# Performance work log

Measured on AMD Instinct MI355X. Metric: run time of the kernel, lower is better.

Reference implementation:

```python
import jax, jax.numpy as jnp
import numpy as np

B, L, N, HID, NH, HD, SH, SW, MH = 1, 512, 2048, 2048, 16, 128, 64, 32, 8192


def _rms(x, w, eps=1e-6):
    return x * jax.lax.rsqrt(jnp.mean(x * x, axis=-1, keepdims=True) + eps) * w


def _adaln(x, emb, W, b, nw):
    e = jax.nn.silu(emb) @ W + b  # [B, 6*hid]
    sh_m, sc_m, g_m, sh_p, sc_p, g_p = jnp.split(e, 6, axis=-1)
    xm = _rms(x, nw) * (1.0 + sc_m[:, None]) + sh_m[:, None]
    return xm, g_m, sh_p, sc_p, g_p


def _rope(x, rope):
    # x: [B, H, S, D], rope: [S, 1, D]
    f = rope[:, 0]  # [S, D]
    cos = jnp.repeat(f[:, 0::2], 2, axis=-1)[None, None]
    sin = jnp.repeat(f[:, 1::2], 2, axis=-1)[None, None]
    xr = x.reshape(*x.shape[:-1], -1, 2)
    x_rot = jnp.stack([-xr[..., 1], xr[..., 0]], axis=-1).reshape(x.shape)
    return x * cos + x_rot * sin


def _sdpa(q, k, v, scale):
    s = jnp.einsum('bhqd,bhkd->bhqk', q, k) * scale
    return jnp.einsum('bhqk,bhkd->bhqd', jax.nn.softmax(s, axis=-1), v)


def _mlp(x, w1, b1, w2, b2):
    return jax.nn.gelu(x @ w1 + b1, approximate=True) @ w2 + b2


def setup_inputs() -> dict:
    key = jax.random.key(0)
    ks = iter(jax.random.split(key, 32))
    r = lambda *s: jax.random.normal(next(ks), s, dtype=jnp.float32) * 0.02
    inp = {
        'txt': jax.random.normal(next(ks), (B, L, HID), dtype=jnp.float32),
        'img': jax.random.normal(next(ks), (B, N, HID), dtype=jnp.float32),
        'vec': jax.random.normal(next(ks), (B, HID), dtype=jnp.float32),
        'rope': jax.random.normal(next(ks), (N, 1, HD), dtype=jnp.float32),
        'sol_temperature': jax.random.uniform(next(ks), (B, 64), dtype=jnp.float32),
        'sol_spatial': jax.random.normal(next(ks), (B, 8, 8), dtype=jnp.float32),
        'ada_img_w': r(HID, 6 * HID), 'ada_img_b': jnp.zeros(6 * HID, jnp.float32), 'ada_img_nw': jnp.ones(HID, jnp.float32),
        'ada_txt_w': r(HID, 6 * HID), 'ada_txt_b': jnp.zeros(6 * HID, jnp.float32), 'ada_txt_nw': jnp.ones(HID, jnp.float32),
        'txt_qkv_w': r(HID, 3 * HID), 'img_qkv_w': r(HID, 3 * HID),
        'txt_out_w': r(HID, HID), 'img_out_w': r(HID, HID),
        'mod_w': r(NH) * 5.0, 'mod_b': r(NH) * 5.0,
        'img_n2_w': jnp.ones(HID, jnp.float32), 'txt_n2_w': jnp.ones(HID, jnp.float32),
        'img_fc1_w': r(HID, MH), 'img_fc1_b': jnp.zeros(MH, jnp.float32),
        'img_fc2_w': r(MH, HID), 'img_fc2_b': jnp.zeros(HID, jnp.float32),
        'txt_fc1_w': r(HID, MH), 'txt_fc1_b': jnp.zeros(MH, jnp.float32),
        'txt_fc2_w': r(MH, HID), 'txt_fc2_b': jnp.zeros(HID, jnp.float32),
        'spatial_h': SH, 'spatial_w': SW,
    }
    return inp


def reference(txt, img, vec, rope, sol_temperature, sol_spatial,
              ada_img_w, ada_img_b, ada_img_nw, ada_txt_w, ada_txt_b, ada_txt_nw,
              txt_qkv_w, img_qkv_w, txt_out_w, img_out_w, mod_w, mod_b,
              img_n2_w, txt_n2_w, img_fc1_w, img_fc1_b, img_fc2_w, img_fc2_b,
              txt_fc1_w, txt_fc1_b, txt_fc2_w, txt_fc2_b, spatial_h, spatial_w):
    b, l, hid = txt.shape
    n = img.shape[1]
    nh = mod_w.shape[0]
    hd = hid // nh
    scale = hd ** (-0.5)

    img_n, img_g, img_shp, img_scp, img_gp = _adaln(img, vec, ada_img_w, ada_img_b, ada_img_nw)
    txt_n, txt_g, txt_shp, txt_scp, txt_gp = _adaln(txt, vec, ada_txt_w, ada_txt_b, ada_txt_nw)

    def qkv(x, w, s):
        p = (x @ w).reshape(b, s, 3, nh, hd).transpose(2, 0, 3, 1, 4)  # [3,B,H,S,D]
        return p[0], p[1], p[2]

    tq, tk, tv = qkv(txt_n, txt_qkv_w, l)
    iq, ik, iv = qkv(img_n, img_qkv_w, n)
    iq = _rope(iq, rope)
    ik = _rope(ik, rope)

    # SOL spatial modulation: bilinear upsample (align_corners=False) + 1x1 conv + exp(clamp)
    sol_up = jax.image.resize(sol_spatial, (b, spatial_h, spatial_w), 'bilinear')
    mod = sol_up[:, None] * mod_w[None, :, None, None] + mod_b[None, :, None, None]
    mod = jnp.exp(jnp.clip(mod, -2.0, 2.0)).reshape(b, nh, n, 1)
    iq = iq * mod
    ik = ik * mod

    k = jnp.concatenate([tk, ik], axis=2)  # [B,H,L+N,D]
    v = jnp.concatenate([tv, iv], axis=2)

    txt_attn = _sdpa(tq, k, v, scale).transpose(0, 2, 1, 3).reshape(b, l, hid) @ txt_out_w

    temp = jnp.clip(jnp.mean(sol_temperature, axis=1, keepdims=True), 0.1)  # [B,1]
    s_eff = jnp.sqrt(scale / temp)[:, :, None, None]  # [B,1,1,1]
    img_attn = _sdpa(iq * s_eff, k * s_eff, v, 1.0).transpose(0, 2, 1, 3).reshape(b, n, hid) @ img_out_w

    txt = txt + txt_g[:, None] * txt_attn
    img = img + img_g[:, None] * img_attn

    txt_in = _rms(txt, txt_n2_w) * (1.0 + txt_scp[:, None]) + txt_shp[:, None]
    img_in = _rms(img, img_n2_w) * (1.0 + img_scp[:, None]) + img_shp[:, None]
    txt = txt + txt_gp[:, None] * _mlp(txt_in, txt_fc1_w, txt_fc1_b, txt_fc2_w, txt_fc2_b)
    img = img + img_gp[:, None] * _mlp(img_in, img_fc1_w, img_fc1_b, img_fc2_w, img_fc2_b)
    return txt, img
```

## Files before the change

kernel.cpp:

```cpp
#include <hip/hip_runtime.h>

typedef short short8 __attribute__((ext_vector_type(8)));
typedef float f32x4 __attribute__((ext_vector_type(4)));

__device__ __forceinline__ unsigned short f2bu(float f) {
  unsigned u = __builtin_bit_cast(unsigned, f);
  u += 0x7fffu + ((u >> 16) & 1u);
  return (unsigned short)(u >> 16);
}

__device__ __forceinline__ float b2f(unsigned short b) {
  unsigned u = (unsigned)b << 16;
  return __builtin_bit_cast(float, u);
}

__device__ __forceinline__ float gelu_t(float x) {
  float x3 = x * x * x;
  float t = tanhf(0.7978845608028654f * (x + 0.044715f * x3));
  return 0.5f * x * (1.f + t);
}

__device__ __forceinline__ void gload16(const void* g, void* l) {
  __builtin_amdgcn_global_load_lds(
      (const __attribute__((address_space(1))) void*)g,
      (__attribute__((address_space(3))) void*)l, 16, 0, 0);
}

__global__ __launch_bounds__(256) void prep_small(
    const float* __restrict__ vec, const float* __restrict__ sol_t,
    float* __restrict__ silu_vec, float* __restrict__ scales) {
  __shared__ float red[4];
  int t = threadIdx.x;
  float v = (t < 64) ? sol_t[t] : 0.f;
#pragma unroll
  for (int o = 32; o > 0; o >>= 1) v += __shfl_down(v, o);
  if ((t & 63) == 0) red[t >> 6] = v;
  __syncthreads();
  if (t == 0) {
    float m = (red[0] + red[1] + red[2] + red[3]) * (1.f / 64.f);
    m = fmaxf(m, 0.1f);
    const float sc = 0.08838834764831845f;
    const float l2e = 1.4426950408889634f;
    scales[0] = sc * l2e;
    scales[1] = sc / m * l2e;
  }
  for (int k = t; k < 2048; k += 256) {
    float x = vec[k];
    silu_vec[k] = x / (1.f + expf(-x));
  }
}

__global__ __launch_bounds__(256) void mod_kernel(
    const float* __restrict__ S, const float* __restrict__ mw,
    const float* __restrict__ mb, float* __restrict__ modb) {
  int idx = blockIdx.x * 256 + threadIdx.x;
  int h = idx >> 11, n = idx & 2047;
  int y = n >> 5, x = n & 31;
  float cy = (y + 0.5f) * 0.125f - 0.5f;
  float cx = (x + 0.5f) * 0.25f - 0.5f;
  int y0 = (int)floorf(cy); float fy = cy - (float)y0;
  int x0 = (int)floorf(cx); float fx = cx - (float)x0;
  int y0c = min(max(y0, 0), 7), y1c = min(max(y0 + 1, 0), 7);
  int x0c = min(max(x0, 0), 7), x1c = min(max(x0 + 1, 0), 7);
  float v = (1.f - fy) * ((1.f - fx) * S[y0c * 8 + x0c] + fx * S[y0c * 8 + x1c]) +
            fy * ((1.f - fx) * S[y1c * 8 + x0c] + fx * S[y1c * 8 + x1c]);
  float t = v * mw[h] + mb[h];
  t = fminf(fmaxf(t, -2.f), 2.f);
  modb[idx] = expf(t);
}

__global__ __launch_bounds__(256) void ada_gemv(
    const float* __restrict__ sv,
    const float* __restrict__ Wi, const float* __restrict__ bi,
    const float* __restrict__ Wt, const float* __restrict__ bt,
    float* __restrict__ ei, float* __restrict__ et) {
  __shared__ float red[4][64];
  const float* W = blockIdx.y ? Wt : Wi;
  const float* bb = blockIdx.y ? bt : bi;
  float* e = blockIdx.y ? et : ei;
  int jl = threadIdx.x & 63, ks = threadIdx.x >> 6;
  int j = blockIdx.x * 64 + jl;
  float acc = 0.f;
  int k0 = ks * 512;
#pragma unroll 4
  for (int k = 0; k < 512; ++k) acc += sv[k0 + k] * W[(size_t)(k0 + k) * 12288 + j];
  red[ks][jl] = acc;
  __syncthreads();
  if (ks == 0) e[j] = red[0][jl] + red[1][jl] + red[2][jl] + red[3][jl] + bb[j];
}

__global__ __launch_bounds__(256) void rmsmod_kernel(
    const float* __restrict__ X, const float* __restrict__ nw,
    const float* __restrict__ e, int sh_off, int sc_off,
    unsigned short* __restrict__ out) {
  __shared__ float red[4];
  int r = blockIdx.x, t = threadIdx.x;
  const float4* xr = reinterpret_cast<const float4*>(X + (size_t)r * 2048);
  float4 v0 = xr[t * 2], v1 = xr[t * 2 + 1];
  float ss = v0.x * v0.x + v0.y * v0.y + v0.z * v0.z + v0.w * v0.w +
             v1.x * v1.x + v1.y * v1.y + v1.z * v1.z + v1.w * v1.w;
#pragma unroll
  for (int o = 32; o > 0; o >>= 1) ss += __shfl_down(ss, o);
  if ((t & 63) == 0) red[t >> 6] = ss;
  __syncthreads();
  float rinv = rsqrtf((red[0] + red[1] + red[2] + red[3]) * (1.f / 2048.f) + 1e-6f);
  int c0 = t * 8;
  float xv[8] = {v0.x, v0.y, v0.z, v0.w, v1.x, v1.y, v1.z, v1.w};
  short8 ov;
#pragma unroll
  for (int i = 0; i < 8; ++i) {
    int c = c0 + i;
    float y = xv[i] * rinv * nw[c] * (1.f + e[sc_off + c]) + e[sh_off + c];
    ov[i] = (short)f2bu(y);
  }
  *reinterpret_cast<short8*>(out + (size_t)r * 2048 + c0) = ov;
}

__global__ __launch_bounds__(256) void transpose_w(
    const float* __restrict__ W, unsigned short* __restrict__ Bt, int K, int N) {
  __shared__ float tile[64][33];
  int n0 = blockIdx.x * 32, k0 = blockIdx.y * 64;
  int tid = threadIdx.x;
  int tx = tid & 31, ty = tid >> 5;
#pragma unroll
  for (int j = 0; j < 8; ++j)
    tile[ty + j * 8][tx] = W[(size_t)(k0 + ty + j * 8) * N + n0 + tx];
  __syncthreads();
  int n = tid >> 3, ks = (tid & 7) * 8;
  unsigned pk[4];
#pragma unroll
  for (int i = 0; i < 4; ++i) {
    float lo = tile[ks + 2 * i][n], hi = tile[ks + 2 * i + 1][n];
    pk[i] = (unsigned)f2bu(lo) | ((unsigned)f2bu(hi) << 16);
  }
  int4 ov = make_int4(pk[0], pk[1], pk[2], pk[3]);
  *reinterpret_cast<int4*>(Bt + (size_t)(n0 + n) * K + k0 + ks) = ov;
}

__global__ __launch_bounds__(256) void transpose_v(
    const unsigned short* __restrict__ V, unsigned short* __restrict__ Vt) {
  __shared__ unsigned short tile[32][33];
  int h = blockIdx.z;
  int s0 = blockIdx.x * 32, d0 = blockIdx.y * 32;
  int tx = threadIdx.x, ty = threadIdx.y;
  const unsigned short* src = V + (size_t)h * 2560 * 128;
  unsigned short* dst = Vt + (size_t)h * 128 * 2560;
#pragma unroll
  for (int j = 0; j < 32; j += 8)
    tile[ty + j][tx] = src[(size_t)(s0 + ty + j) * 128 + d0 + tx];
  __syncthreads();
#pragma unroll
  for (int j = 0; j < 32; j += 8)
    dst[(size_t)(d0 + ty + j) * 2560 + s0 + tx] = tile[tx][ty + j];
}

struct GemmP {
  const unsigned short *A, *Bt_t, *Bt_i;
  float* C;
  unsigned short* Cb;
  const float *bias_t, *bias_i;
  const float *rope, *modb;
  unsigned short *q_txt, *q_img, *k_cat, *v_cat;
  const float* scales;
  int Mb_t;
  int N, K, KS;
};

template <int EPI>
__global__ __launch_bounds__(256) void gemm2(GemmP p) {
  __shared__ int4 sA[2][128 * 8];
  __shared__ int4 sB[2][128 * 8];
  const int NB = gridDim.x, MBT = gridDim.y;
  int nwg = NB * MBT;
  int orig = blockIdx.y * NB + blockIdx.x;
  int qq = nwg >> 3, rr = nwg & 7, xcd = orig & 7, base = orig >> 3;
  int sw = (xcd < rr ? xcd * (qq + 1) : rr * (qq + 1) + (xcd - rr) * qq) + base;
  int bx = sw / MBT, by = sw % MBT;
  const bool is_t = by < p.Mb_t;
  const unsigned short* Bt = is_t ? p.Bt_t : p.Bt_i;
  const int m0 = by * 128, n0 = bx * 128;
  const int z = blockIdx.z;
  const int Kz = p.K / p.KS, kbeg = z * Kz, kend = kbeg + Kz;
  const int tid = threadIdx.x;
  const int w = tid >> 6, l = tid & 63, lr = l & 15, lg = l >> 4;
  const int wm = (w >> 1) * 64, wn = (w & 1) * 64;
  f32x4 acc[4][4] = {};
  const int4* Ag = reinterpret_cast<const int4*>(p.A);
  const int4* Bg = reinterpret_cast<const int4*>(Bt);
  const int K8 = p.K >> 3;
  int srow[4], sch[4];
#pragma unroll
  for (int i = 0; i < 4; ++i) {
    int s = i * 256 + tid;
    srow[i] = s >> 3;
    sch[i] = (s & 7) ^ (srow[i] & 7);
  }
  {
    int kc = kbeg >> 3;
#pragma unroll
    for (int i = 0; i < 4; ++i) {
      gload16(&Ag[(size_t)(m0 + srow[i]) * K8 + kc + sch[i]], &sA[0][i * 256 + w * 64]);
      gload16(&Bg[(size_t)(n0 + srow[i]) * K8 + kc + sch[i]], &sB[0][i * 256 + w * 64]);
    }
  }
  asm volatile("s_waitcnt vmcnt(0)" ::: "memory");
  __builtin_amdgcn_sched_barrier(0);
  __builtin_amdgcn_s_barrier();
  int cur = 0;
  for (int k0 = kbeg; k0 < kend; k0 += 64) {
    if (k0 + 64 < kend) {
      int kc = (k0 + 64) >> 3;
#pragma unroll
      for (int i = 0; i < 4; ++i) {
        gload16(&Ag[(size_t)(m0 + srow[i]) * K8 + kc + sch[i]], &sA[cur ^ 1][i * 256 + w * 64]);
        gload16(&Bg[(size_t)(n0 + srow[i]) * K8 + kc + sch[i]], &sB[cur ^ 1][i * 256 + w * 64]);
      }
      __builtin_amdgcn_sched_barrier(0);
    }
    const short8* pA = reinterpret_cast<const short8*>(sA[cur]);
    const short8* pB = reinterpret_cast<const short8*>(sB[cur]);
#pragma unroll
    for (int kk = 0; kk < 2; ++kk) {
      short8 af[4], bf[4];
#pragma unroll
      for (int m = 0; m < 4; ++m) {
        int row = wm + m * 16 + lr;
        af[m] = pA[row * 8 + ((kk * 4 + lg) ^ (row & 7))];
      }
#pragma unroll
      for (int n = 0; n < 4; ++n) {
        int row = wn + n * 16 + lr;
        bf[n] = pB[row * 8 + ((kk * 4 + lg) ^ (row & 7))];
      }
#pragma unroll
      for (int m = 0; m < 4; ++m)
#pragma unroll
        for (int n = 0; n < 4; ++n)
          acc[m][n] = __builtin_amdgcn_mfma_f32_16x16x32_bf16(af[m], bf[n], acc[m][n], 0, 0, 0);
    }
    asm volatile("s_waitcnt vmcnt(0)" ::: "memory");
    __builtin_amdgcn_sched_barrier(0);
    __builtin_amdgcn_s_barrier();
    cur ^= 1;
  }
  if (EPI == 0) {
    float* C = p.C + (size_t)z * MBT * 128 * p.N;
#pragma unroll
    for (int m = 0; m < 4; ++m)
#pragma unroll
      for (int n = 0; n < 4; ++n)
#pragma unroll
        for (int j = 0; j < 4; ++j) {
          int r = m0 + wm + m * 16 + lg * 4 + j;
          int cc = n0 + wn + n * 16 + lr;
          C[(size_t)r * p.N + cc] = acc[m][n][j];
        }
  } else if (EPI == 1) {
    const float* bias = is_t ? p.bias_t : p.bias_i;
#pragma unroll
    for (int n = 0; n < 4; ++n) {
      int cc = n0 + wn + n * 16 + lr;
      float bv = bias[cc];
#pragma unroll
      for (int m = 0; m < 4; ++m)
#pragma unroll
        for (int j = 0; j < 4; ++j) {
          int r = m0 + wm + m * 16 + lg * 4 + j;
          p.Cb[(size_t)r * p.N + cc] = f2bu(gelu_t(acc[m][n][j] + bv));
        }
    }
  } else {
    int sel = bx >> 4, h = bx & 15;
#pragma unroll
    for (int n = 0; n < 4; ++n) {
      int d = wn + n * 16 + lr;
#pragma unroll
      for (int m = 0; m < 4; ++m)
#pragma unroll
        for (int j = 0; j < 4; ++j) {
          int r = m0 + wm + m * 16 + lg * 4 + j;
          float v = acc[m][n][j];
          if (is_t) {
            if (sel == 0) p.q_txt[((size_t)h * 512 + r) * 128 + d] = f2bu(v * p.scales[0]);
            else if (sel == 1) p.k_cat[((size_t)h * 2560 + r) * 128 + d] = f2bu(v);
            else p.v_cat[((size_t)h * 2560 + r) * 128 + d] = f2bu(v);
          } else {
            int s = r - 512;
            if (sel == 2) {
              p.v_cat[((size_t)h * 2560 + r) * 128 + d] = f2bu(v);
            } else {
              float c = p.rope[s * 128 + (d & ~1)];
              float sn = p.rope[s * 128 + (d | 1)];
              float part = __shfl_xor(v, 1);
              float vr = (d & 1) ? v * c + part * sn : v * c - part * sn;
              vr *= p.modb[h * 2048 + s];
              if (sel == 0) p.q_img[((size_t)h * 2048 + s) * 128 + d] = f2bu(vr * p.scales[1]);
              else p.k_cat[((size_t)h * 2560 + r) * 128 + d] = f2bu(vr);
            }
          }
        }
    }
  }
}

__global__ __launch_bounds__(256, 4) void attn_kernel(
    const unsigned short* __restrict__ q_txt, const unsigned short* __restrict__ q_img,
    const unsigned short* __restrict__ Kc, const unsigned short* __restrict__ Vt,
    unsigned short* __restrict__ Op, float* __restrict__ ml) {
  __shared__ __align__(16) char RAW[40960];
  int4* sK = reinterpret_cast<int4*>(RAW);
  int4* sV = reinterpret_cast<int4*>(RAW + 16384);
  int4* sP = reinterpret_cast<int4*>(RAW + 32768);
  unsigned short* osh = reinterpret_cast<unsigned short*>(RAW);
  const int tid = threadIdx.x, w = tid >> 6, l = tid & 63, lr = l & 15, lg = l >> 4;
  const int bx = blockIdx.x, h = blockIdx.y, z = blockIdx.z;
  const bool is_t = bx < 8;
  const int orow = is_t ? bx * 64 : 512 + (bx - 8) * 64;
  const unsigned short* Qp = is_t ? q_txt + ((size_t)h * 512 + bx * 64) * 128
                                  : q_img + ((size_t)h * 2048 + (bx - 8) * 64) * 128;
  short8 aq[4];
#pragma unroll
  for (int ds = 0; ds < 4; ++ds) {
    int row = w * 16 + lr;
    aq[ds] = *reinterpret_cast<const short8*>(Qp + (size_t)row * 128 + ds * 32 + lg * 8);
  }
  const int4* Kg = reinterpret_cast<const int4*>(Kc + (size_t)h * 2560 * 128);
  const int4* Vg = reinterpret_cast<const int4*>(Vt + (size_t)h * 128 * 2560);
  const short8* pK = reinterpret_cast<const short8*>(sK);
  const short8* pV = reinterpret_cast<const short8*>(sV);
  const short8* pP = reinterpret_cast<const short8*>(sP);
  unsigned short* sPb = reinterpret_cast<unsigned short*>(sP);
  int krow[4], kch[4], vrow[4], vch[4];
#pragma unroll
  for (int i = 0; i < 4; ++i) {
    int s = i * 256 + tid;
    krow[i] = s >> 4; kch[i] = (s & 15) ^ (krow[i] & 7);
    vrow[i] = s >> 3; vch[i] = (s & 7) ^ (vrow[i] & 7);
  }
  short8 ones8;
#pragma unroll
  for (int i = 0; i < 8; ++i) ones8[i] = (short)0x3F80;

  f32x4 oacc[8] = {};
  f32x4 oacc_l = {};
  float m_run[4];
#pragma unroll
  for (int j = 0; j < 4; ++j) m_run[j] = -1e30f;

  const int kbeg = z * 10, kend = kbeg + 10;
#pragma unroll
  for (int i = 0; i < 4; ++i)
    gload16(&Kg[(size_t)(kbeg * 64 + krow[i]) * 16 + kch[i]], &sK[i * 256 + w * 64]);
#pragma unroll
  for (int i = 0; i < 4; ++i)
    gload16(&Vg[(size_t)vrow[i] * 320 + kbeg * 8 + vch[i]], &sV[i * 256 + w * 64]);

  for (int kt = kbeg; kt < kend; ++kt) {
    asm volatile("s_waitcnt vmcnt(4)" ::: "memory");
    __builtin_amdgcn_sched_barrier(0);
    __builtin_amdgcn_s_barrier();
    f32x4 sacc[4] = {};
    __builtin_amdgcn_s_setprio(1);
#pragma unroll
    for (int ds = 0; ds < 4; ++ds) {
      short8 bk[4];
#pragma unroll
      for (int n = 0; n < 4; ++n) {
        int row = n * 16 + lr;
        bk[n] = pK[row * 16 + ((ds * 4 + lg) ^ (row & 7))];
      }
#pragma unroll
      for (int n = 0; n < 4; ++n)
        sacc[n] = __builtin_amdgcn_mfma_f32_16x16x32_bf16(aq[ds], bk[n], sacc[n], 0, 0, 0);
    }
    __builtin_amdgcn_s_setprio(0);
    __builtin_amdgcn_s_barrier();
    if (kt + 1 < kend) {
#pragma unroll
      for (int i = 0; i < 4; ++i)
        gload16(&Kg[(size_t)((kt + 1) * 64 + krow[i]) * 16 + kch[i]], &sK[i * 256 + w * 64]);
    }
    float corr_[4];
    bool grow_any = false;
#pragma unroll
    for (int j = 0; j < 4; ++j) {
      float mx = fmaxf(fmaxf(sacc[0][j], sacc[1][j]), fmaxf(sacc[2][j], sacc[3][j]));
      mx = fmaxf(mx, __shfl_xor(mx, 1));
      mx = fmaxf(mx, __shfl_xor(mx, 2));
      mx = fmaxf(mx, __shfl_xor(mx, 4));
      mx = fmaxf(mx, __shfl_xor(mx, 8));
      bool grow = mx > m_run[j] + 11.0f;
      grow_any |= grow;
      float mn = grow ? mx : m_run[j];
      corr_[j] = exp2f(m_run[j] - mn);
      m_run[j] = mn;
      int prow = w * 16 + lg * 4 + j;
#pragma unroll
      for (int n = 0; n < 4; ++n) {
        float pp = exp2f(sacc[n][j] - mn);
        int col = n * 16 + lr;
        sPb[prow * 64 + (((col >> 3) ^ (prow & 7)) << 3) + (col & 7)] = f2bu(pp);
      }
    }
    if (__any(grow_any)) {
#pragma unroll
      for (int n = 0; n < 8; ++n)
#pragma unroll
        for (int j = 0; j < 4; ++j) oacc[n][j] *= corr_[j];
#pragma unroll
      for (int j = 0; j < 4; ++j) oacc_l[j] *= corr_[j];
    }
    if (kt + 1 < kend) {
      asm volatile("s_waitcnt vmcnt(4)" ::: "memory");
    } else {
      asm volatile("s_waitcnt vmcnt(0)" ::: "memory");
    }
    __builtin_amdgcn_sched_barrier(0);
    __builtin_amdgcn_s_barrier();
    __builtin_amdgcn_s_setprio(1);
#pragma unroll
    for (int kk = 0; kk < 2; ++kk) {
      short8 ap, bv[8];
      {
        int row = w * 16 + lr;
        ap = pP[row * 8 + ((kk * 4 + lg) ^ (row & 7))];
      }
#pragma unroll
      for (int n = 0; n < 8; ++n) {
        int row = n * 16 + lr;
        bv[n] = pV[row * 8 + ((kk * 4 + lg) ^ (row & 7))];
      }
#pragma unroll
      for (int n = 0; n < 8; ++n)
        oacc[n] = __builtin_amdgcn_mfma_f32_16x16x32_bf16(ap, bv[n], oacc[n], 0, 0, 0);
      oacc_l = __builtin_amdgcn_mfma_f32_16x16x32_bf16(ap, ones8, oacc_l, 0, 0, 0);
    }
    __builtin_amdgcn_s_setprio(0);
    __builtin_amdgcn_s_barrier();
    if (kt + 1 < kend) {
#pragma unroll
      for (int i = 0; i < 4; ++i)
        gload16(&Vg[(size_t)vrow[i] * 320 + (kt + 1) * 8 + vch[i]], &sV[i * 256 + w * 64]);
    }
  }
  const size_t zbase = (size_t)z * 40960 + (size_t)h * 2560 + orow;
  __syncthreads();
#pragma unroll
  for (int j = 0; j < 4; ++j) {
    int row = w * 16 + lg * 4 + j;
#pragma unroll
    for (int n = 0; n < 8; ++n)
      osh[row * 136 + n * 16 + lr] = f2bu(oacc[n][j]);
    if (lr == 0) {
      ml[(zbase + row) * 2] = m_run[j];
      ml[(zbase + row) * 2 + 1] = oacc_l[j];
    }
  }
  __syncthreads();
  {
    int row = tid >> 2, c0 = (tid & 3) * 32;
#pragma unroll
    for (int i = 0; i < 4; ++i)
      *reinterpret_cast<short8*>(Op + (zbase + row) * 128 + c0 + i * 8) =
          *reinterpret_cast<const short8*>(osh + row * 136 + c0 + i * 8);
  }
}

__global__ __launch_bounds__(256) void attn_merge(
    const unsigned short* __restrict__ Op, const float* __restrict__ ml,
    unsigned short* __restrict__ ao) {
  int gid = blockIdx.x * 256 + threadIdx.x;
  int rid = gid >> 5, d0 = (gid & 31) * 4;
  int h = rid / 2560;
  int r = rid - h * 2560;
  float M = -1e30f;
#pragma unroll
  for (int z = 0; z < 4; ++z) M = fmaxf(M, ml[((size_t)z * 40960 + rid) * 2]);
  float L = 0.f, o0 = 0.f, o1 = 0.f, o2 = 0.f, o3 = 0.f;
#pragma unroll
  for (int z = 0; z < 4; ++z) {
    size_t sidx = (size_t)z * 40960 + rid;
    float mz = ml[sidx * 2], lz = ml[sidx * 2 + 1];
    float wgt = exp2f(mz - M);
    L += wgt * lz;
    ushort4 v = *reinterpret_cast<const ushort4*>(Op + sidx * 128 + d0);
    o0 += wgt * b2f(v.x); o1 += wgt * b2f(v.y);
    o2 += wgt * b2f(v.z); o3 += wgt * b2f(v.w);
  }
  float inv = 1.f / L;
  ushort4 ov;
  ov.x = f2bu(o0 * inv); ov.y = f2bu(o1 * inv);
  ov.z = f2bu(o2 * inv); ov.w = f2bu(o3 * inv);
  *reinterpret_cast<ushort4*>(ao + (size_t)r * 2048 + h * 128 + d0) = ov;
}

__global__ __launch_bounds__(256) void residual1(
    const float4* __restrict__ X, const float4* __restrict__ P0,
    const float4* __restrict__ P1, const float* __restrict__ e,
    float4* __restrict__ out, int total4) {
  int stride = gridDim.x * 256;
  for (int i = blockIdx.x * 256 + threadIdx.x; i < total4; i += stride) {
    int c = (i * 4) & 2047;
    float4 g = *reinterpret_cast<const float4*>(e + 4096 + c);
    float4 x = X[i], p0 = P0[i], p1 = P1[i], o;
    o.x = x.x + g.x * (p0.x + p1.x); o.y = x.y + g.y * (p0.y + p1.y);
    o.z = x.z + g.z * (p0.z + p1.z); o.w = x.w + g.w * (p0.w + p1.w);
    out[i] = o;
  }
}

__global__ __launch_bounds__(256) void residual2(
    const float4* __restrict__ P0, const float4* __restrict__ P1,
    const float* __restrict__ b2, const float* __restrict__ e,
    float4* __restrict__ out, int total4) {
  int stride = gridDim.x * 256;
  for (int i = blockIdx.x * 256 + threadIdx.x; i < total4; i += stride) {
    int c = (i * 4) & 2047;
    float4 g = *reinterpret_cast<const float4*>(e + 10240 + c);
    float4 bb = *reinterpret_cast<const float4*>(b2 + c);
    float4 p0 = P0[i], p1 = P1[i], o = out[i];
    o.x += g.x * (p0.x + p1.x + bb.x); o.y += g.y * (p0.y + p1.y + bb.y);
    o.z += g.z * (p0.z + p1.z + bb.z); o.w += g.w * (p0.w + p1.w + bb.w);
    out[i] = o;
  }
}

extern "C" void kernel_launch(void* const* d_in, const int* in_sizes, int n_in,
                              void* d_out, int out_size, void* d_ws, size_t ws_size,
                              hipStream_t stream) {
  (void)in_sizes; (void)n_in; (void)out_size; (void)ws_size;
  const float* txt = (const float*)d_in[0];
  const float* img = (const float*)d_in[1];
  const float* vec = (const float*)d_in[2];
  const float* rope = (const float*)d_in[3];
  const float* sol_t = (const float*)d_in[4];
  const float* sol_s = (const float*)d_in[5];
  const float* ada_img_w = (const float*)d_in[6];
  const float* ada_img_b = (const float*)d_in[7];
  const float* ada_img_nw = (const float*)d_in[8];
  const float* ada_txt_w = (const float*)d_in[9];
  const float* ada_txt_b = (const float*)d_in[10];
  const float* ada_txt_nw = (const float*)d_in[11];
  const float* txt_qkv_w = (const float*)d_in[12];
  const float* img_qkv_w = (const float*)d_in[13];
  const float* txt_out_w = (const float*)d_in[14];
  const float* img_out_w = (const float*)d_in[15];
  const float* mod_w = (const float*)d_in[16];
  const float* mod_b = (const float*)d_in[17];
  const float* img_n2_w = (const float*)d_in[18];
  const float* txt_n2_w = (const float*)d_in[19];
  const float* img_fc1_w = (const float*)d_in[20];
  const float* img_fc1_b = (const float*)d_in[21];
  const float* img_fc2_w = (const float*)d_in[22];
  const float* img_fc2_b = (const float*)d_in[23];
  const float* txt_fc1_w = (const float*)d_in[24];
  const float* txt_fc1_b = (const float*)d_in[25];
  const float* txt_fc2_w = (const float*)d_in[26];
  const float* txt_fc2_b = (const float*)d_in[27];
  float* out = (float*)d_out;
  float* out_img = out + (size_t)512 * 2048;
  char* ws = (char*)d_ws;

  const size_t MB = 1 << 20;
  float* silu_vec = (float*)(ws + 0);
  float* scales = (float*)(ws + 8192);
  float* modb = (float*)(ws + 16384);
  float* e_img = (float*)(ws + 147456);
  float* e_txt = (float*)(ws + 196608);
  unsigned short* wt0 = (unsigned short*)(ws + 1 * MB);
  unsigned short* wt1 = (unsigned short*)(ws + 33 * MB);
  unsigned short* Opart = (unsigned short*)(ws + 1 * MB);
  float* mlbuf = (float*)(ws + 42 * MB);
  unsigned short* actA = (unsigned short*)(ws + 65 * MB);
  char* attn_base = ws + 75 * MB;
  unsigned short* q_txt = (unsigned short*)(attn_base);
  unsigned short* q_img = (unsigned short*)(attn_base + 2 * MB);
  unsigned short* k_cat = (unsigned short*)(attn_base + 10 * MB);
  unsigned short* v_cat = (unsigned short*)(attn_base + 20 * MB);
  unsigned short* vT = (unsigned short*)(attn_base + 30 * MB);
  unsigned short* ao = (unsigned short*)(attn_base + 40 * MB);
  unsigned short* actB = (unsigned short*)attn_base;
  float* Cbuf = (float*)(ws + 125 * MB);
  const size_t PSTR = (size_t)2560 * 2048;

  prep_small<<<1, 256, 0, stream>>>(vec, sol_t, silu_vec, scales);
  mod_kernel<<<128, 256, 0, stream>>>(sol_s, mod_w, mod_b, modb);
  ada_gemv<<<dim3(192, 2), 256, 0, stream>>>(silu_vec, ada_img_w, ada_img_b,
                                             ada_txt_w, ada_txt_b, e_img, e_txt);
  rmsmod_kernel<<<512, 256, 0, stream>>>(txt, ada_txt_nw, e_txt, 0, 2048, actA);
  rmsmod_kernel<<<2048, 256, 0, stream>>>(img, ada_img_nw, e_img, 0, 2048,
                                          actA + (size_t)512 * 2048);
  transpose_w<<<dim3(192, 32), 256, 0, stream>>>(txt_qkv_w, wt0, 2048, 6144);
  transpose_w<<<dim3(192, 32), 256, 0, stream>>>(img_qkv_w, wt1, 2048, 6144);
  {
    GemmP p = {actA, wt0, wt1, nullptr, nullptr, nullptr, nullptr,
               rope, modb, q_txt, q_img, k_cat, v_cat, scales, 4, 6144, 2048, 1};
    gemm2<2><<<dim3(48, 20, 1), 256, 0, stream>>>(p);
  }
  transpose_v<<<dim3(80, 4, 16), dim3(32, 8), 0, stream>>>(v_cat, vT);
  attn_kernel<<<dim3(40, 16, 4), 256, 0, stream>>>(q_txt, q_img, k_cat, vT, Opart, mlbuf);
  attn_merge<<<5120, 256, 0, stream>>>(Opart, mlbuf, ao);
  transpose_w<<<dim3(64, 32), 256, 0, stream>>>(txt_out_w, wt0, 2048, 2048);
  transpose_w<<<dim3(64, 32), 256, 0, stream>>>(img_out_w, wt1, 2048, 2048);
  {
    GemmP p = {ao, wt0, wt1, Cbuf, nullptr, nullptr, nullptr,
               nullptr, nullptr, nullptr, nullptr, nullptr, nullptr, nullptr, 4, 2048, 2048, 2};
    gemm2<0><<<dim3(16, 20, 2), 256, 0, stream>>>(p);
  }
  residual1<<<512, 256, 0, stream>>>((const float4*)txt, (const float4*)Cbuf,
                                     (const float4*)(Cbuf + PSTR), e_txt,
                                     (float4*)out, 512 * 2048 / 4);
  residual1<<<1024, 256, 0, stream>>>((const float4*)img,
                                      (const float4*)(Cbuf + (size_t)512 * 2048),
                                      (const float4*)(Cbuf + PSTR + (size_t)512 * 2048), e_img,
                                      (float4*)out_img, 2048 * 2048 / 4);
  rmsmod_kernel<<<512, 256, 0, stream>>>(out, txt_n2_w, e_txt, 6144, 8192, actA);
  rmsmod_kernel<<<2048, 256, 0, stream>>>(out_img, img_n2_w, e_img, 6144, 8192,
                                          actA + (size_t)512 * 2048);
  transpose_w<<<dim3(256, 32), 256, 0, stream>>>(txt_fc1_w, wt0, 2048, 8192);
  transpose_w<<<dim3(256, 32), 256, 0, stream>>>(img_fc1_w, wt1, 2048, 8192);
  {
    GemmP p = {actA, wt0, wt1, nullptr, actB, txt_fc1_b, img_fc1_b,
               nullptr, nullptr, nullptr, nullptr, nullptr, nullptr, nullptr, 4, 8192, 2048, 1};
    gemm2<1><<<dim3(64, 20, 1), 256, 0, stream>>>(p);
  }
  transpose_w<<<dim3(64, 128), 256, 0, stream>>>(txt_fc2_w, wt0, 8192, 2048);
  transpose_w<<<dim3(64, 128), 256, 0, stream>>>(img_fc2_w, wt1, 8192, 2048);
  {
    GemmP p = {actB, wt0, wt1, Cbuf, nullptr, nullptr, nullptr,
               nullptr, nullptr, nullptr, nullptr, nullptr, nullptr, nullptr, 4, 2048, 8192, 2};
    gemm2<0><<<dim3(16, 20, 2), 256, 0, stream>>>(p);
  }
  residual2<<<512, 256, 0, stream>>>((const float4*)Cbuf, (const float4*)(Cbuf + PSTR),
                                     txt_fc2_b, e_txt, (float4*)out, 512 * 2048 / 4);
  residual2<<<1024, 256, 0, stream>>>((const float4*)(Cbuf + (size_t)512 * 2048),
                                      (const float4*)(Cbuf + PSTR + (size_t)512 * 2048),
                                      img_fc2_b, e_img, (float4*)out_img, 2048 * 2048 / 4);
}
```

Measured before the change: 853.7 us.

## Stage QKV GEMM epilogue through LDS for vectorized stores; XCD-swizzle attention blocks

```diff
diff --git a/kernel.cpp b/kernel.cpp
--- a/kernel.cpp
+++ b/kernel.cpp
@@ -168,8 +168,9 @@
 
 template <int EPI>
 __global__ __launch_bounds__(256) void gemm2(GemmP p) {
-  __shared__ int4 sA[2][128 * 8];
-  __shared__ int4 sB[2][128 * 8];
+  __shared__ __align__(16) char GRAW[65536];
+  int4* sAb = reinterpret_cast<int4*>(GRAW);
+  int4* sBb = reinterpret_cast<int4*>(GRAW + 32768);
   const int NB = gridDim.x, MBT = gridDim.y;
   int nwg = NB * MBT;
   int orig = blockIdx.y * NB + blockIdx.x;
@@ -199,8 +200,8 @@
     int kc = kbeg >> 3;
 #pragma unroll
     for (int i = 0; i < 4; ++i) {
-      gload16(&Ag[(size_t)(m0 + srow[i]) * K8 + kc + sch[i]], &sA[0][i * 256 + w * 64]);
-      gload16(&Bg[(size_t)(n0 + srow[i]) * K8 + kc + sch[i]], &sB[0][i * 256 + w * 64]);
+      gload16(&Ag[(size_t)(m0 + srow[i]) * K8 + kc + sch[i]], &sAb[i * 256 + w * 64]);
+      gload16(&Bg[(size_t)(n0 + srow[i]) * K8 + kc + sch[i]], &sBb[i * 256 + w * 64]);
     }
   }
   asm volatile("s_waitcnt vmcnt(0)" ::: "memory");
@@ -210,15 +211,16 @@
   for (int k0 = kbeg; k0 < kend; k0 += 64) {
     if (k0 + 64 < kend) {
       int kc = (k0 + 64) >> 3;
+      int nb = (cur ^ 1) * 1024;
 #pragma unroll
       for (int i = 0; i < 4; ++i) {
-        gload16(&Ag[(size_t)(m0 + srow[i]) * K8 + kc + sch[i]], &sA[cur ^ 1][i * 256 + w * 64]);
-        gload16(&Bg[(size_t)(n0 + srow[i]) * K8 + kc + sch[i]], &sB[cur ^ 1][i * 256 + w * 64]);
+        gload16(&Ag[(size_t)(m0 + srow[i]) * K8 + kc + sch[i]], &sAb[nb + i * 256 + w * 64]);
+        gload16(&Bg[(size_t)(n0 + srow[i]) * K8 + kc + sch[i]], &sBb[nb + i * 256 + w * 64]);
       }
       __builtin_amdgcn_sched_barrier(0);
     }
-    const short8* pA = reinterpret_cast<const short8*>(sA[cur]);
-    const short8* pB = reinterpret_cast<const short8*>(sB[cur]);
+    const short8* pA = reinterpret_cast<const short8*>(sAb + cur * 1024);
+    const short8* pB = reinterpret_cast<const short8*>(sBb + cur * 1024);
 #pragma unroll
     for (int kk = 0; kk < 2; ++kk) {
       short8 af[4], bf[4];
@@ -270,35 +272,73 @@
         }
     }
   } else {
+    unsigned short* osh = reinterpret_cast<unsigned short*>(GRAW);
+#pragma unroll
+    for (int m = 0; m < 4; ++m)
+#pragma unroll
+      for (int n = 0; n < 4; ++n)
+#pragma unroll
+        for (int j = 0; j < 4; ++j) {
+          int row = wm + m * 16 + lg * 4 + j;
+          int col = wn + n * 16 + lr;
+          osh[row * 136 + col] = f2bu(acc[m][n][j]);
+        }
+    __syncthreads();
     int sel = bx >> 4, h = bx & 15;
-#pragma unroll
-    for (int n = 0; n < 4; ++n) {
-      int d = wn + n * 16 + lr;
-#pragma unroll
-      for (int m = 0; m < 4; ++m)
-#pragma unroll
-        for (int j = 0; j < 4; ++j) {
-          int r = m0 + wm + m * 16 + lg * 4 + j;
-          float v = acc[m][n][j];
-          if (is_t) {
-            if (sel == 0) p.q_txt[((size_t)h * 512 + r) * 128 + d] = f2bu(v * p.scales[0]);
-            else if (sel == 1) p.k_cat[((size_t)h * 2560 + r) * 128 + d] = f2bu(v);
-            else p.v_cat[((size_t)h * 2560 + r) * 128 + d] = f2bu(v);
-          } else {
-            int s = r - 512;
-            if (sel == 2) {
-              p.v_cat[((size_t)h * 2560 + r) * 128 + d] = f2bu(v);
-            } else {
-              float c = p.rope[s * 128 + (d & ~1)];
-              float sn = p.rope[s * 128 + (d | 1)];
-              float part = __shfl_xor(v, 1);
-              float vr = (d & 1) ? v * c + part * sn : v * c - part * sn;
-              vr *= p.modb[h * 2048 + s];
-              if (sel == 0) p.q_img[((size_t)h * 2048 + s) * 128 + d] = f2bu(vr * p.scales[1]);
-              else p.k_cat[((size_t)h * 2560 + r) * 128 + d] = f2bu(vr);
-            }
+    int row = tid >> 1, d0 = (tid & 1) * 64;
+    int r = m0 + row;
+    const unsigned short* src = osh + row * 136 + d0;
+    if (is_t) {
+      if (sel == 0) {
+        float qs = p.scales[0];
+        unsigned short* dst = p.q_txt + ((size_t)h * 512 + r) * 128 + d0;
+#pragma unroll
+        for (int i = 0; i < 8; ++i) {
+          short8 v = *reinterpret_cast<const short8*>(src + i * 8);
+          short8 o;
+#pragma unroll
+          for (int t = 0; t < 8; ++t)
+            o[t] = (short)f2bu(b2f((unsigned short)v[t]) * qs);
+          *reinterpret_cast<short8*>(dst + i * 8) = o;
+        }
+      } else {
+        unsigned short* dst =
+            (sel == 1 ? p.k_cat : p.v_cat) + ((size_t)h * 2560 + r) * 128 + d0;
+#pragma unroll
+        for (int i = 0; i < 8; ++i)
+          *reinterpret_cast<short8*>(dst + i * 8) =
+              *reinterpret_cast<const short8*>(src + i * 8);
+      }
+    } else {
+      int s = r - 512;
+      if (sel == 2) {
+        unsigned short* dst = p.v_cat + ((size_t)h * 2560 + r) * 128 + d0;
+#pragma unroll
+        for (int i = 0; i < 8; ++i)
+          *reinterpret_cast<short8*>(dst + i * 8) =
+              *reinterpret_cast<const short8*>(src + i * 8);
+      } else {
+        float mv = p.modb[h * 2048 + s];
+        float qs = (sel == 0) ? p.scales[1] * mv : mv;
+        const float2* rp = reinterpret_cast<const float2*>(p.rope + (size_t)s * 128 + d0);
+        unsigned short* dst = (sel == 0)
+            ? p.q_img + ((size_t)h * 2048 + s) * 128 + d0
+            : p.k_cat + ((size_t)h * 2560 + r) * 128 + d0;
+#pragma unroll
+        for (int i = 0; i < 8; ++i) {
+          short8 v = *reinterpret_cast<const short8*>(src + i * 8);
+          short8 o;
+#pragma unroll
+          for (int t = 0; t < 4; ++t) {
+            float2 cs = rp[i * 4 + t];
+            float e = b2f((unsigned short)v[2 * t]);
+            float od = b2f((unsigned short)v[2 * t + 1]);
+            o[2 * t] = (short)f2bu((e * cs.x - od * cs.y) * qs);
+            o[2 * t + 1] = (short)f2bu((od * cs.x + e * cs.y) * qs);
           }
+          *reinterpret_cast<short8*>(dst + i * 8) = o;
         }
+      }
     }
   }
 }
@@ -313,7 +353,11 @@
   int4* sP = reinterpret_cast<int4*>(RAW + 32768);
   unsigned short* osh = reinterpret_cast<unsigned short*>(RAW);
   const int tid = threadIdx.x, w = tid >> 6, l = tid & 63, lr = l & 15, lg = l >> 4;
-  const int bx = blockIdx.x, h = blockIdx.y, z = blockIdx.z;
+  int flat = blockIdx.x + 40 * (blockIdx.y + 16 * blockIdx.z);
+  int sw = (flat & 7) * 320 + (flat >> 3);
+  const int bx = sw % 40;
+  int hz = sw / 40;
+  const int h = hz & 15, z = hz >> 4;
   const bool is_t = bx < 8;
   const int orow = is_t ? bx * 64 : 512 + (bx - 8) * 64;
   const unsigned short* Qp = is_t ? q_txt + ((size_t)h * 512 + bx * 64) * 128
```

Result: faster. 731.1 us (-14.4%).
